# Performance work log

Measured on AMD Instinct MI355X. Metric: run time of the kernel, lower is better.

Reference implementation:

```python
import jax, jax.numpy as jnp
import numpy as np

WS = 7          # window_size
SHIFT = 3       # shift_size
HEADS = 3
DIM = 96
HID = 384       # mlp_ratio * dim
EPS = 1e-5


def _rel_pos_index(ws):
    coords = np.stack(np.meshgrid(np.arange(ws), np.arange(ws), indexing='ij')).reshape(2, -1)
    rel = (coords[:, :, None] - coords[:, None, :]).transpose(1, 2, 0)
    rel[:, :, 0] += ws - 1
    rel[:, :, 1] += ws - 1
    rel[:, :, 0] *= 2 * ws - 1
    return jnp.asarray(rel.sum(-1))  # (ws*ws, ws*ws) int

REL_IDX = _rel_pos_index(WS)


def _shift_mask(H, W):
    # standard Swin SW-MSA mask: (nW, N, N), 0 / -100
    img = np.zeros((H, W), dtype=np.int32)
    cnt = 0
    for h in (slice(0, -WS), slice(-WS, -SHIFT), slice(-SHIFT, None)):
        for w in (slice(0, -WS), slice(-WS, -SHIFT), slice(-SHIFT, None)):
            img[h, w] = cnt
            cnt += 1
    win = img.reshape(H // WS, WS, W // WS, WS).transpose(0, 2, 1, 3).reshape(-1, WS * WS)
    diff = win[:, None, :] - win[:, :, None]
    return jnp.asarray(np.where(diff != 0, -100.0, 0.0).astype(np.float32))


def _ln(x, g, b):
    m = x.mean(-1, keepdims=True)
    v = ((x - m) ** 2).mean(-1, keepdims=True)
    return (x - m) * jax.lax.rsqrt(v + EPS) * g + b


def setup_inputs() -> dict:
    key = jax.random.key(0)
    ks = jax.random.split(key, 12)
    B, H, W, C = 16, 112, 112, DIM
    s = 0.02
    return {
        'x': jax.random.normal(ks[0], (B, H * W, C), jnp.float32),
        'mask': _shift_mask(H, W),
        'norm1_g': jnp.ones((C,), jnp.float32),
        'norm1_b': jnp.zeros((C,), jnp.float32),
        'qkv_w': jax.random.normal(ks[1], (3 * C, C), jnp.float32) * s,
        'qkv_b': jnp.zeros((3 * C,), jnp.float32),
        'rel_bias_table': jax.random.normal(ks[2], ((2 * WS - 1) ** 2, HEADS), jnp.float32) * s,
        'proj_w': jax.random.normal(ks[3], (C, C), jnp.float32) * s,
        'proj_b': jnp.zeros((C,), jnp.float32),
        'norm2_g': jnp.ones((C,), jnp.float32),
        'norm2_b': jnp.zeros((C,), jnp.float32),
        'fc1_w': jax.random.normal(ks[4], (HID, C), jnp.float32) * s,
        'fc1_b': jnp.zeros((HID,), jnp.float32),
        'fc2_w': jax.random.normal(ks[5], (C, HID), jnp.float32) * s,
        'fc2_b': jnp.zeros((C,), jnp.float32),
        'H': 112,
        'W': 112,
    }


def reference(x, mask, norm1_g, norm1_b, qkv_w, qkv_b, rel_bias_table, proj_w,
              proj_b, norm2_g, norm2_b, fc1_w, fc1_b, fc2_w, fc2_b, H, W):
    B, L, C = x.shape
    N = WS * WS
    hd = C // HEADS
    scale = hd ** -0.5
    nh, nw = H // WS, W // WS

    shortcut = x
    h = _ln(x, norm1_g, norm1_b).reshape(B, H, W, C)
    # cyclic shift
    h = jnp.roll(h, (-SHIFT, -SHIFT), axis=(1, 2))
    # window partition -> (B*nW, N, C)
    xw = h.reshape(B, nh, WS, nw, WS, C).transpose(0, 1, 3, 2, 4, 5).reshape(-1, N, C)
    B_ = xw.shape[0]

    qkv = (xw @ qkv_w.T + qkv_b).reshape(B_, N, 3, HEADS, hd).transpose(2, 0, 3, 1, 4)
    q, k, v = qkv[0], qkv[1], qkv[2]          # (B_, heads, N, hd)
    attn = jnp.einsum('bhnd,bhmd->bhnm', q * scale, k)

    bias = rel_bias_table[REL_IDX.reshape(-1)].reshape(N, N, HEADS).transpose(2, 0, 1)
    attn = attn + bias[None]

    nW = mask.shape[0]
    attn = attn.reshape(B_ // nW, nW, HEADS, N, N) + mask[None, :, None]
    attn = jax.nn.softmax(attn.reshape(B_, HEADS, N, N), axis=-1)

    out = jnp.einsum('bhnm,bhmd->bhnd', attn, v).transpose(0, 2, 1, 3).reshape(B_, N, C)
    out = out @ proj_w.T + proj_b

    # window reverse + reverse shift
    out = out.reshape(B, nh, nw, WS, WS, C).transpose(0, 1, 3, 2, 4, 5).reshape(B, H, W, C)
    out = jnp.roll(out, (SHIFT, SHIFT), axis=(1, 2)).reshape(B, L, C)

    x = shortcut + out
    y = _ln(x, norm2_g, norm2_b)
    y = jax.nn.gelu(y @ fc1_w.T + fc1_b, approximate=False)
    y = y @ fc2_w.T + fc2_b
    return x + y
```

## Files before the change

### kernel.cpp

```cpp
#include <hip/hip_runtime.h>
#include <hip/hip_bf16.h>
#include <math.h>


typedef __attribute__((ext_vector_type(8))) short bfrag8;
typedef __attribute__((ext_vector_type(4))) float f32x4;

__device__ __forceinline__ float bf2f(unsigned short u){
  union { unsigned int i; float f; } c; c.i = ((unsigned int)u) << 16; return c.f;
}
__device__ __forceinline__ unsigned short f2bf(float f){
  __hip_bfloat16 h = __float2bfloat16(f);
  union { __hip_bfloat16 h; unsigned short u; } c; c.h = h; return c.u;
}
__device__ __forceinline__ float gelu_f(float x){
  float x2 = x * x;
  float z  = x + 0.044715f * x * x2;
  float u  = __expf(-1.5957691f * z);
  return x / (1.f + u);
}

__device__ __forceinline__ int swz32(int r, int c){
  return r * 32 + (c ^ (((r ^ (r >> 2)) & 3) << 3));
}
__device__ __forceinline__ int swz64(int r, int c){
  return r * 64 + (c ^ (((r ^ (r >> 3)) & 7) << 3));
}

__device__ __forceinline__ int win_to_img(int r){
  int win = r / 49, n = r - win * 49;
  int b  = win >> 8, wi = win & 255;
  int wh = wi >> 4,  ww = wi & 15;
  int i  = n / 7,    j  = n - i * 7;
  int hs = wh * 7 + i + 3; if (hs >= 112) hs -= 112;
  int ws = ww * 7 + j + 3; if (ws >= 112) ws -= 112;
  return b * 12544 + hs * 112 + ws;
}

__global__ __launch_bounds__(256) void cvt_all_kernel(
    const float* __restrict__ s1, unsigned short* __restrict__ d1,
    const float* __restrict__ s2, unsigned short* __restrict__ d2,
    const float* __restrict__ s3, unsigned short* __restrict__ d3,
    const float* __restrict__ s4, unsigned short* __restrict__ d4)
{
  int i = blockIdx.x * 256 + threadIdx.x;
  if      (i < 36864)  d1[i]          = f2bf(s1[i]);
  else if (i < 73728)  d2[i - 36864]  = f2bf(s2[i - 36864]);
  else if (i < 101376) d3[i - 73728]  = f2bf(s3[i - 73728]);
  else if (i < 110592) d4[i - 101376] = f2bf(s4[i - 101376]);
}

__global__ __launch_bounds__(256) void cb_kernel(
    const float* __restrict__ relt, const float* __restrict__ mask,
    float* __restrict__ cbt)
{
  int idx = blockIdx.x * 256 + threadIdx.x;
  int wh = idx >> 12;
  int w = wh / 3, h = wh - w * 3;
  int rem = idx & 4095;
  int mt = rem >> 10, nt = (rem >> 8) & 3, qd = (rem >> 6) & 3;
  int ln = (rem >> 2) & 15, r = rem & 3;
  int m = mt * 16 + qd * 4 + r, n = nt * 16 + ln;
  float v;
  if (m < 49 && n < 49){
    int i1 = m / 7, j1 = m - i1 * 7;
    int i2 = n / 7, j2 = n - i2 * 7;
    int ridx = (i1 - i2 + 6) * 13 + (j1 - j2 + 6);
    v = relt[ridx * 3 + h] + mask[w * 2401 + m * 49 + n];
  } else if (n >= 49) v = -10000.0f;
  else v = 0.0f;
  cbt[idx] = v;
}

__global__ __launch_bounds__(256, 4) void fused_win_kernel(
    const float* __restrict__ x,
    const float* __restrict__ g1, const float* __restrict__ b1n,
    const unsigned short* __restrict__ wqkv, const float* __restrict__ bqkv,
    const float* __restrict__ cbt,
    const unsigned short* __restrict__ wproj, const float* __restrict__ bproj,
    unsigned short* __restrict__ x2)
{
  __shared__ unsigned short L[18944];

  int win = blockIdx.x, tid = threadIdx.x;
  const float scale = 0.17677669529663687f;

  {
    int r = tid >> 2, part = tid & 3;
    if (r < 49){
      int gr = win_to_img(win * 49 + r);
      const float* rowp = x + (size_t)gr * 96 + part * 24;
      float v[24]; float s = 0.f, q = 0.f;
      #pragma unroll
      for (int c = 0; c < 24; c++){ v[c] = rowp[c]; s += v[c]; q += v[c] * v[c]; }
      s += __shfl_xor(s, 1); q += __shfl_xor(q, 1);
      s += __shfl_xor(s, 2); q += __shfl_xor(q, 2);
      float mean = s * (1.f / 96.f);
      float rs = rsqrtf(q * (1.f / 96.f) - mean * mean + 1e-5f);
      #pragma unroll
      for (int c = 0; c < 24; c++){
        int cc = part * 24 + c;
        L[r * 104 + cc] = f2bf((v[c] - mean) * rs * g1[cc] + b1n[cc]);
      }
    } else {
      #pragma unroll
      for (int c = 0; c < 24; c++) L[r * 104 + part * 24 + c] = 0;
    }
  }
  __syncthreads();

  int wave = tid >> 6, lane = tid & 63;
  int ln = lane & 15, qd = lane >> 4;

  bfrag8 af[4][3];
  #pragma unroll
  for (int mt = 0; mt < 4; mt++)
    #pragma unroll
    for (int k3 = 0; k3 < 3; k3++)
      af[mt][k3] = *reinterpret_cast<const bfrag8*>(
          &L[(mt * 16 + ln) * 104 + k3 * 32 + qd * 8]);
  __syncthreads();

  {
    int nct = (wave < 2) ? 5 : 4;
    for (int i = 0; i < nct; i++){
      int nt = wave + i * 4;
      int col = nt * 16 + ln;
      const unsigned short* wp = wqkv + (size_t)col * 96 + qd * 8;
      bfrag8 B0 = *reinterpret_cast<const bfrag8*>(wp);
      bfrag8 B1 = *reinterpret_cast<const bfrag8*>(wp + 32);
      bfrag8 B2 = *reinterpret_cast<const bfrag8*>(wp + 64);
      float bs = bqkv[col];
      #pragma unroll
      for (int mt = 0; mt < 4; mt++){
        f32x4 acc = {0.f, 0.f, 0.f, 0.f};
        acc = __builtin_amdgcn_mfma_f32_16x16x32_bf16(af[mt][0], B0, acc, 0, 0, 0);
        acc = __builtin_amdgcn_mfma_f32_16x16x32_bf16(af[mt][1], B1, acc, 0, 0, 0);
        acc = __builtin_amdgcn_mfma_f32_16x16x32_bf16(af[mt][2], B2, acc, 0, 0, 0);
        if (nt < 6){
          int hh = col >> 5, d = col & 31;
          #pragma unroll
          for (int r = 0; r < 4; r++){
            int m = mt * 16 + qd * 4 + r;
            L[6656 + hh * 4096 + swz32(m, d)] = f2bf((acc[r] + bs) * scale);
          }
        } else if (nt < 12){
          int cc = col - 96; int hh = cc >> 5, d = cc & 31;
          #pragma unroll
          for (int r = 0; r < 4; r++){
            int m = mt * 16 + qd * 4 + r;
            L[6656 + hh * 4096 + 2048 + swz32(m, d)] = f2bf(acc[r] + bs);
          }
        } else {
          int cc = col - 192; int hh = cc >> 5, d = cc & 31;
          #pragma unroll
          for (int r = 0; r < 4; r++){
            int m = mt * 16 + qd * 4 + r;
            L[hh * 2048 + swz64(d, m)] = f2bf(acc[r] + bs);
          }
        }
      }
    }
  }
  __syncthreads();

  int h = wave;
  if (wave < 3){
    bfrag8 qf[4];
    #pragma unroll
    for (int mt = 0; mt < 4; mt++)
      qf[mt] = *reinterpret_cast<const bfrag8*>(
          &L[6656 + h * 4096 + swz32(mt * 16 + ln, qd * 8)]);
    f32x4 sf[4][4];
    #pragma unroll
    for (int nt = 0; nt < 4; nt++){
      bfrag8 kf = *reinterpret_cast<const bfrag8*>(
          &L[6656 + h * 4096 + 2048 + swz32(nt * 16 + ln, qd * 8)]);
      #pragma unroll
      for (int mt = 0; mt < 4; mt++){
        f32x4 z = {0.f, 0.f, 0.f, 0.f};
        sf[mt][nt] = __builtin_amdgcn_mfma_f32_16x16x32_bf16(qf[mt], kf, z, 0, 0, 0);
      }
    }
    const float* cbh = cbt + ((size_t)(win & 255) * 3 + h) * 4096;
    #pragma unroll
    for (int mt = 0; mt < 4; mt++)
      #pragma unroll
      for (int nt = 0; nt < 4; nt++){
        f32x4 cv = *reinterpret_cast<const f32x4*>(
            cbh + mt * 1024 + nt * 256 + qd * 64 + ln * 4);
        #pragma unroll
        for (int r = 0; r < 4; r++) sf[mt][nt][r] += cv[r];
      }
    #pragma unroll
    for (int mt = 0; mt < 4; mt++){
      float mx[4], sm[4];
      #pragma unroll
      for (int r = 0; r < 4; r++)
        mx[r] = fmaxf(fmaxf(sf[mt][0][r], sf[mt][1][r]),
                      fmaxf(sf[mt][2][r], sf[mt][3][r]));
      #pragma unroll
      for (int r = 0; r < 4; r++)
        #pragma unroll
        for (int off = 1; off < 16; off <<= 1)
          mx[r] = fmaxf(mx[r], __shfl_xor(mx[r], off));
      #pragma unroll
      for (int r = 0; r < 4; r++){
        float e0 = __expf(sf[mt][0][r] - mx[r]);
        float e1 = __expf(sf[mt][1][r] - mx[r]);
        float e2 = __expf(sf[mt][2][r] - mx[r]);
        float e3 = __expf(sf[mt][3][r] - mx[r]);
        sf[mt][0][r] = e0; sf[mt][1][r] = e1; sf[mt][2][r] = e2; sf[mt][3][r] = e3;
        sm[r] = e0 + e1 + e2 + e3;
      }
      #pragma unroll
      for (int r = 0; r < 4; r++)
        #pragma unroll
        for (int off = 1; off < 16; off <<= 1)
          sm[r] += __shfl_xor(sm[r], off);
      #pragma unroll
      for (int r = 0; r < 4; r++){
        float inv = 1.f / sm[r];
        int m = mt * 16 + qd * 4 + r;
        #pragma unroll
        for (int nt = 0; nt < 4; nt++)
          L[6656 + h * 4096 + swz64(m, nt * 16 + ln)] = f2bf(sf[mt][nt][r] * inv);
      }
    }

    f32x4 of[4][2];
    #pragma unroll
    for (int mt = 0; mt < 4; mt++)
      #pragma unroll
      for (int dt = 0; dt < 2; dt++) of[mt][dt] = (f32x4){0.f, 0.f, 0.f, 0.f};
    #pragma unroll
    for (int k2 = 0; k2 < 2; k2++){
      bfrag8 vf[2];
      #pragma unroll
      for (int dt = 0; dt < 2; dt++)
        vf[dt] = *reinterpret_cast<const bfrag8*>(
            &L[h * 2048 + swz64(dt * 16 + ln, k2 * 32 + qd * 8)]);
      #pragma unroll
      for (int mt = 0; mt < 4; mt++){
        bfrag8 pf = *reinterpret_cast<const bfrag8*>(
            &L[6656 + h * 4096 + swz64(mt * 16 + ln, k2 * 32 + qd * 8)]);
        #pragma unroll
        for (int dt = 0; dt < 2; dt++)
          of[mt][dt] = __builtin_amdgcn_mfma_f32_16x16x32_bf16(pf, vf[dt], of[mt][dt], 0, 0, 0);
      }
    }
    #pragma unroll
    for (int mt = 0; mt < 4; mt++)
      #pragma unroll
      for (int r = 0; r < 4; r++){
        int m = mt * 16 + qd * 4 + r;
        #pragma unroll
        for (int dt = 0; dt < 2; dt++)
          L[h * 2048 + swz32(m, dt * 16 + ln)] = f2bf(of[mt][dt][r]);
      }
  }
  __syncthreads();

  {
    int rh = wave >> 1, nh = wave & 1;
    bfrag8 ap[2][3];
    #pragma unroll
    for (int mt2 = 0; mt2 < 2; mt2++)
      #pragma unroll
      for (int k3 = 0; k3 < 3; k3++)
        ap[mt2][k3] = *reinterpret_cast<const bfrag8*>(
            &L[k3 * 2048 + swz32(rh * 32 + mt2 * 16 + ln, qd * 8)]);
    f32x4 pacc[2][3];
    #pragma unroll
    for (int nt3 = 0; nt3 < 3; nt3++){
      int col = (nh * 3 + nt3) * 16 + ln;
      const unsigned short* wp = wproj + (size_t)col * 96 + qd * 8;
      bfrag8 B0 = *reinterpret_cast<const bfrag8*>(wp);
      bfrag8 B1 = *reinterpret_cast<const bfrag8*>(wp + 32);
      bfrag8 B2 = *reinterpret_cast<const bfrag8*>(wp + 64);
      #pragma unroll
      for (int mt2 = 0; mt2 < 2; mt2++){
        f32x4 acc = {0.f, 0.f, 0.f, 0.f};
        acc = __builtin_amdgcn_mfma_f32_16x16x32_bf16(ap[mt2][0], B0, acc, 0, 0, 0);
        acc = __builtin_amdgcn_mfma_f32_16x16x32_bf16(ap[mt2][1], B1, acc, 0, 0, 0);
        acc = __builtin_amdgcn_mfma_f32_16x16x32_bf16(ap[mt2][2], B2, acc, 0, 0, 0);
        pacc[mt2][nt3] = acc;
      }
    }
    #pragma unroll
    for (int mt2 = 0; mt2 < 2; mt2++)
      #pragma unroll
      for (int r = 0; r < 4; r++){
        int m = rh * 32 + mt2 * 16 + qd * 4 + r;
        if (m < 49){
          int gi = win_to_img(win * 49 + m);
          #pragma unroll
          for (int nt3 = 0; nt3 < 3; nt3++){
            int col = (nh * 3 + nt3) * 16 + ln;
            x2[(size_t)gi * 96 + col] =
                f2bf(pacc[mt2][nt3][r] + bproj[col] + x[(size_t)gi * 96 + col]);
          }
        }
      }
  }
}

__global__ __launch_bounds__(384, 4) void mlp_mfma_kernel(
    const unsigned short* __restrict__ x2,
    const float* __restrict__ g, const float* __restrict__ b,
    const unsigned short* __restrict__ w1, const float* __restrict__ b1,
    const unsigned short* __restrict__ w2, const float* __restrict__ b2,
    float* __restrict__ out)
{
  __shared__ unsigned short S[25088];
  unsigned short* As = S;
  unsigned short* Hs = S;
  int tid = threadIdx.x;
  int row0 = blockIdx.x * 64;

  {
    int r = tid / 6, c = (tid - r * 6) * 16;
    *reinterpret_cast<bfrag8*>(&As[r * 104 + c]) =
        *reinterpret_cast<const bfrag8*>(x2 + (size_t)(row0 + r) * 96 + c);
    *reinterpret_cast<bfrag8*>(&As[r * 104 + c + 8]) =
        *reinterpret_cast<const bfrag8*>(x2 + (size_t)(row0 + r) * 96 + c + 8);
  }
  __syncthreads();
  if (tid < 256){
    int rr = tid >> 2, part = tid & 3;
    float v[24]; float s = 0.f, q = 0.f;
    #pragma unroll
    for (int c = 0; c < 24; c++){
      v[c] = bf2f(As[rr * 104 + part * 24 + c]);
      s += v[c]; q += v[c] * v[c];
    }
    s += __shfl_xor(s, 1); q += __shfl_xor(q, 1);
    s += __shfl_xor(s, 2); q += __shfl_xor(q, 2);
    float mean = s * (1.f / 96.f);
    float rs = rsqrtf(q * (1.f / 96.f) - mean * mean + 1e-5f);
    #pragma unroll
    for (int c = 0; c < 24; c++){
      int cc = part * 24 + c;
      As[rr * 104 + cc] = f2bf((v[c] - mean) * rs * g[cc] + b[cc]);
    }
  }
  __syncthreads();

  int wave = tid / 64, lane = tid & 63;
  int ln = lane & 15, qd = lane >> 4;

  bfrag8 af[4][3];
  #pragma unroll
  for (int mt = 0; mt < 4; mt++)
    #pragma unroll
    for (int k3 = 0; k3 < 3; k3++)
      af[mt][k3] = *reinterpret_cast<const bfrag8*>(
          &As[(mt * 16 + ln) * 104 + k3 * 32 + qd * 8]);
  __syncthreads();

  for (int i = 0; i < 4; i++){
    int ntl = wave + i * 6;
    int col = ntl * 16 + ln;
    const unsigned short* wp = w1 + (size_t)col * 96 + qd * 8;
    bfrag8 B0 = *reinterpret_cast<const bfrag8*>(wp);
    bfrag8 B1 = *reinterpret_cast<const bfrag8*>(wp + 32);
    bfrag8 B2 = *reinterpret_cast<const bfrag8*>(wp + 64);
    float bias = b1[col];
    #pragma unroll
    for (int mt = 0; mt < 4; mt++){
      f32x4 a = {0.f, 0.f, 0.f, 0.f};
      a = __builtin_amdgcn_mfma_f32_16x16x32_bf16(af[mt][0], B0, a, 0, 0, 0);
      a = __builtin_amdgcn_mfma_f32_16x16x32_bf16(af[mt][1], B1, a, 0, 0, 0);
      a = __builtin_amdgcn_mfma_f32_16x16x32_bf16(af[mt][2], B2, a, 0, 0, 0);
      #pragma unroll
      for (int r = 0; r < 4; r++)
        Hs[(mt * 16 + qd * 4 + r) * 392 + col] = f2bf(gelu_f(a[r] + bias));
    }
  }
  __syncthreads();

  f32x4 acc[4];
  #pragma unroll
  for (int mt = 0; mt < 4; mt++) acc[mt] = (f32x4){0.f, 0.f, 0.f, 0.f};
  for (int k2 = 0; k2 < 12; k2++){
    bfrag8 B = *reinterpret_cast<const bfrag8*>(
        w2 + (size_t)(wave * 16 + ln) * 384 + k2 * 32 + qd * 8);
    #pragma unroll
    for (int mt = 0; mt < 4; mt++){
      bfrag8 p = *reinterpret_cast<const bfrag8*>(
          &Hs[(mt * 16 + ln) * 392 + k2 * 32 + qd * 8]);
      acc[mt] = __builtin_amdgcn_mfma_f32_16x16x32_bf16(p, B, acc[mt], 0, 0, 0);
    }
  }
  {
    int col = wave * 16 + ln;
    float bias = b2[col];
    #pragma unroll
    for (int mt = 0; mt < 4; mt++)
      #pragma unroll
      for (int r = 0; r < 4; r++){
        int grow = row0 + mt * 16 + qd * 4 + r;
        out[(size_t)grow * 96 + col] =
            acc[mt][r] + bias + bf2f(x2[(size_t)grow * 96 + col]);
      }
  }
}

extern "C" void kernel_launch(void* const* d_in, const int* in_sizes, int n_in,
                              void* d_out, int out_size, void* d_ws, size_t ws_size,
                              hipStream_t stream)
{
  const float* x      = (const float*)d_in[0];
  const float* mask   = (const float*)d_in[1];
  const float* n1g    = (const float*)d_in[2];
  const float* n1b    = (const float*)d_in[3];
  const float* qkv_w  = (const float*)d_in[4];
  const float* qkv_b  = (const float*)d_in[5];
  const float* relt   = (const float*)d_in[6];
  const float* proj_w = (const float*)d_in[7];
  const float* proj_b = (const float*)d_in[8];
  const float* n2g    = (const float*)d_in[9];
  const float* n2b    = (const float*)d_in[10];
  const float* fc1_w  = (const float*)d_in[11];
  const float* fc1_b  = (const float*)d_in[12];
  const float* fc2_w  = (const float*)d_in[13];
  const float* fc2_b  = (const float*)d_in[14];
  float* outp = (float*)d_out;
  (void)in_sizes; (void)n_in; (void)out_size; (void)ws_size; (void)mask;

  const size_t M = 200704;
  char* ws = (char*)d_ws;
  unsigned short* x2     = (unsigned short*)ws;
  size_t o = M * 96 * 2;
  unsigned short* w1bf   = (unsigned short*)(ws + o); o += 384 * 96 * 2;
  unsigned short* w2bf   = (unsigned short*)(ws + o); o += 96 * 384 * 2;
  unsigned short* wqkvbf = (unsigned short*)(ws + o); o += 288 * 96 * 2;
  unsigned short* wprojbf= (unsigned short*)(ws + o); o += 96 * 96 * 2;
  float*          cbuf   = (float*)(ws + o); o += (size_t)256 * 3 * 4096 * 4;

  cvt_all_kernel<<<432, 256, 0, stream>>>(
      fc1_w, w1bf, fc2_w, w2bf, qkv_w, wqkvbf, proj_w, wprojbf);
  cb_kernel<<<12288, 256, 0, stream>>>(relt, mask, cbuf);
  fused_win_kernel<<<4096, 256, 0, stream>>>(
      x, n1g, n1b, wqkvbf, qkv_b, cbuf, wprojbf, proj_b, x2);
  mlp_mfma_kernel<<<3136, 384, 0, stream>>>(
      x2, n2g, n2b, w1bf, fc1_b, w2bf, fc2_b, outp);
}
```

Measured before the change: 335.3 us.

## Spread window attention over all waves, use exp2 softmax, retune LDS swizzles

```diff
diff --git a/kernel.cpp b/kernel.cpp
--- a/kernel.cpp
+++ b/kernel.cpp
@@ -6,6 +6,8 @@
 typedef __attribute__((ext_vector_type(8))) short bfrag8;
 typedef __attribute__((ext_vector_type(4))) float f32x4;
 
+#define LOG2E 1.4426950408889634f
+
 __device__ __forceinline__ float bf2f(unsigned short u){
   union { unsigned int i; float f; } c; c.i = ((unsigned int)u) << 16; return c.f;
 }
@@ -14,17 +16,21 @@
   union { __hip_bfloat16 h; unsigned short u; } c; c.h = h; return c.u;
 }
 __device__ __forceinline__ float gelu_f(float x){
+  const float c1 = -2.302208198f, c2 = -0.1029432397f;
   float x2 = x * x;
-  float z  = x + 0.044715f * x * x2;
-  float u  = __expf(-1.5957691f * z);
-  return x / (1.f + u);
+  float t  = __builtin_fmaf(x2, c2, c1);
+  float u  = exp2f(x * t);
+  return x * __builtin_amdgcn_rcpf(1.f + u);
 }
 
 __device__ __forceinline__ int swz32(int r, int c){
-  return r * 32 + (c ^ (((r ^ (r >> 2)) & 3) << 3));
+  return r * 32 + (c ^ (((r + (r >> 2)) & 3) << 3));
 }
 __device__ __forceinline__ int swz64(int r, int c){
-  return r * 64 + (c ^ (((r ^ (r >> 3)) & 7) << 3));
+  return r * 64 + (c ^ (((r ^ (r >> 1)) & 7) << 3));
+}
+__device__ __forceinline__ int hswz(int r, int c){
+  return r * 392 + (c ^ (((r >> 3) & 3) << 4));
 }
 
 __device__ __forceinline__ int win_to_img(int r){
@@ -37,24 +43,24 @@
   return b * 12544 + hs * 112 + ws;
 }
 
-__global__ __launch_bounds__(256) void cvt_all_kernel(
+__global__ __launch_bounds__(256) void prep_kernel(
     const float* __restrict__ s1, unsigned short* __restrict__ d1,
     const float* __restrict__ s2, unsigned short* __restrict__ d2,
     const float* __restrict__ s3, unsigned short* __restrict__ d3,
-    const float* __restrict__ s4, unsigned short* __restrict__ d4)
-{
-  int i = blockIdx.x * 256 + threadIdx.x;
-  if      (i < 36864)  d1[i]          = f2bf(s1[i]);
-  else if (i < 73728)  d2[i - 36864]  = f2bf(s2[i - 36864]);
-  else if (i < 101376) d3[i - 73728]  = f2bf(s3[i - 73728]);
-  else if (i < 110592) d4[i - 101376] = f2bf(s4[i - 101376]);
-}
-
-__global__ __launch_bounds__(256) void cb_kernel(
+    const float* __restrict__ s4, unsigned short* __restrict__ d4,
     const float* __restrict__ relt, const float* __restrict__ mask,
     float* __restrict__ cbt)
 {
-  int idx = blockIdx.x * 256 + threadIdx.x;
+  int bid = blockIdx.x;
+  if (bid < 432){
+    int i = bid * 256 + threadIdx.x;
+    if      (i < 36864)  d1[i]          = f2bf(s1[i]);
+    else if (i < 73728)  d2[i - 36864]  = f2bf(s2[i - 36864]);
+    else if (i < 101376) d3[i - 73728]  = f2bf(s3[i - 73728]);
+    else if (i < 110592) d4[i - 101376] = f2bf(s4[i - 101376]);
+    return;
+  }
+  int idx = (bid - 432) * 256 + threadIdx.x;
   int wh = idx >> 12;
   int w = wh / 3, h = wh - w * 3;
   int rem = idx & 4095;
@@ -66,7 +72,7 @@
     int i1 = m / 7, j1 = m - i1 * 7;
     int i2 = n / 7, j2 = n - i2 * 7;
     int ridx = (i1 - i2 + 6) * 13 + (j1 - j2 + 6);
-    v = relt[ridx * 3 + h] + mask[w * 2401 + m * 49 + n];
+    v = (relt[ridx * 3 + h] + mask[w * 2401 + m * 49 + n]) * LOG2E;
   } else if (n >= 49) v = -10000.0f;
   else v = 0.0f;
   cbt[idx] = v;
@@ -83,7 +89,7 @@
   __shared__ unsigned short L[18944];
 
   int win = blockIdx.x, tid = threadIdx.x;
-  const float scale = 0.17677669529663687f;
+  const float qscale = (float)(0.17677669529663687 * 1.4426950408889634);
 
   {
     int r = tid >> 2, part = tid & 3;
@@ -142,7 +148,7 @@
           #pragma unroll
           for (int r = 0; r < 4; r++){
             int m = mt * 16 + qd * 4 + r;
-            L[6656 + hh * 4096 + swz32(m, d)] = f2bf((acc[r] + bs) * scale);
+            L[6656 + hh * 4096 + swz32(m, d)] = f2bf((acc[r] + bs) * qscale);
           }
         } else if (nt < 12){
           int cc = col - 96; int hh = cc >> 5, d = cc & 31;
@@ -164,100 +170,93 @@
   }
   __syncthreads();
 
-  int h = wave;
-  if (wave < 3){
-    bfrag8 qf[4];
-    #pragma unroll
-    for (int mt = 0; mt < 4; mt++)
-      qf[mt] = *reinterpret_cast<const bfrag8*>(
-          &L[6656 + h * 4096 + swz32(mt * 16 + ln, qd * 8)]);
-    f32x4 sf[4][4];
+  int u0 = wave * 3;
+  bfrag8 qf[3];
+  f32x4 sf[3][4];
+  #pragma unroll
+  for (int i = 0; i < 3; i++){
+    int u = u0 + i, hh = u >> 2, mt = u & 3;
+    qf[i] = *reinterpret_cast<const bfrag8*>(
+        &L[6656 + hh * 4096 + swz32(mt * 16 + ln, qd * 8)]);
     #pragma unroll
     for (int nt = 0; nt < 4; nt++){
       bfrag8 kf = *reinterpret_cast<const bfrag8*>(
-          &L[6656 + h * 4096 + 2048 + swz32(nt * 16 + ln, qd * 8)]);
-      #pragma unroll
-      for (int mt = 0; mt < 4; mt++){
-        f32x4 z = {0.f, 0.f, 0.f, 0.f};
-        sf[mt][nt] = __builtin_amdgcn_mfma_f32_16x16x32_bf16(qf[mt], kf, z, 0, 0, 0);
-      }
-    }
-    const float* cbh = cbt + ((size_t)(win & 255) * 3 + h) * 4096;
-    #pragma unroll
-    for (int mt = 0; mt < 4; mt++)
-      #pragma unroll
-      for (int nt = 0; nt < 4; nt++){
-        f32x4 cv = *reinterpret_cast<const f32x4*>(
-            cbh + mt * 1024 + nt * 256 + qd * 64 + ln * 4);
-        #pragma unroll
-        for (int r = 0; r < 4; r++) sf[mt][nt][r] += cv[r];
-      }
-    #pragma unroll
-    for (int mt = 0; mt < 4; mt++){
-      float mx[4], sm[4];
-      #pragma unroll
-      for (int r = 0; r < 4; r++)
-        mx[r] = fmaxf(fmaxf(sf[mt][0][r], sf[mt][1][r]),
-                      fmaxf(sf[mt][2][r], sf[mt][3][r]));
-      #pragma unroll
-      for (int r = 0; r < 4; r++)
-        #pragma unroll
-        for (int off = 1; off < 16; off <<= 1)
-          mx[r] = fmaxf(mx[r], __shfl_xor(mx[r], off));
-      #pragma unroll
-      for (int r = 0; r < 4; r++){
-        float e0 = __expf(sf[mt][0][r] - mx[r]);
-        float e1 = __expf(sf[mt][1][r] - mx[r]);
-        float e2 = __expf(sf[mt][2][r] - mx[r]);
-        float e3 = __expf(sf[mt][3][r] - mx[r]);
-        sf[mt][0][r] = e0; sf[mt][1][r] = e1; sf[mt][2][r] = e2; sf[mt][3][r] = e3;
-        sm[r] = e0 + e1 + e2 + e3;
-      }
-      #pragma unroll
-      for (int r = 0; r < 4; r++)
-        #pragma unroll
-        for (int off = 1; off < 16; off <<= 1)
-          sm[r] += __shfl_xor(sm[r], off);
-      #pragma unroll
-      for (int r = 0; r < 4; r++){
-        float inv = 1.f / sm[r];
-        int m = mt * 16 + qd * 4 + r;
-        #pragma unroll
-        for (int nt = 0; nt < 4; nt++)
-          L[6656 + h * 4096 + swz64(m, nt * 16 + ln)] = f2bf(sf[mt][nt][r] * inv);
-      }
-    }
-
-    f32x4 of[4][2];
-    #pragma unroll
-    for (int mt = 0; mt < 4; mt++)
-      #pragma unroll
-      for (int dt = 0; dt < 2; dt++) of[mt][dt] = (f32x4){0.f, 0.f, 0.f, 0.f};
+          &L[6656 + hh * 4096 + 2048 + swz32(nt * 16 + ln, qd * 8)]);
+      f32x4 z = {0.f, 0.f, 0.f, 0.f};
+      sf[i][nt] = __builtin_amdgcn_mfma_f32_16x16x32_bf16(qf[i], kf, z, 0, 0, 0);
+    }
+    const float* cbh = cbt + ((size_t)(win & 255) * 3 + hh) * 4096 + mt * 1024;
+    #pragma unroll
+    for (int nt = 0; nt < 4; nt++){
+      f32x4 cv = *reinterpret_cast<const f32x4*>(cbh + nt * 256 + qd * 64 + ln * 4);
+      #pragma unroll
+      for (int r = 0; r < 4; r++) sf[i][nt][r] += cv[r];
+    }
+  }
+  __syncthreads();
+
+  f32x4 of[3][2];
+  #pragma unroll
+  for (int i = 0; i < 3; i++){
+    int u = u0 + i, hh = u >> 2, mt = u & 3;
+    float mx[4], sm[4];
+    #pragma unroll
+    for (int r = 0; r < 4; r++)
+      mx[r] = fmaxf(fmaxf(sf[i][0][r], sf[i][1][r]),
+                    fmaxf(sf[i][2][r], sf[i][3][r]));
+    #pragma unroll
+    for (int r = 0; r < 4; r++)
+      #pragma unroll
+      for (int off = 1; off < 16; off <<= 1)
+        mx[r] = fmaxf(mx[r], __shfl_xor(mx[r], off));
+    #pragma unroll
+    for (int r = 0; r < 4; r++){
+      float e0 = exp2f(sf[i][0][r] - mx[r]);
+      float e1 = exp2f(sf[i][1][r] - mx[r]);
+      float e2 = exp2f(sf[i][2][r] - mx[r]);
+      float e3 = exp2f(sf[i][3][r] - mx[r]);
+      sf[i][0][r] = e0; sf[i][1][r] = e1; sf[i][2][r] = e2; sf[i][3][r] = e3;
+      sm[r] = e0 + e1 + e2 + e3;
+    }
+    #pragma unroll
+    for (int r = 0; r < 4; r++)
+      #pragma unroll
+      for (int off = 1; off < 16; off <<= 1)
+        sm[r] += __shfl_xor(sm[r], off);
+    #pragma unroll
+    for (int r = 0; r < 4; r++){
+      float inv = __builtin_amdgcn_rcpf(sm[r]);
+      int m = mt * 16 + qd * 4 + r;
+      #pragma unroll
+      for (int nt = 0; nt < 4; nt++)
+        L[6656 + hh * 4096 + swz64(m, nt * 16 + ln)] = f2bf(sf[i][nt][r] * inv);
+    }
+    of[i][0] = (f32x4){0.f, 0.f, 0.f, 0.f};
+    of[i][1] = (f32x4){0.f, 0.f, 0.f, 0.f};
     #pragma unroll
     for (int k2 = 0; k2 < 2; k2++){
-      bfrag8 vf[2];
+      bfrag8 pf = *reinterpret_cast<const bfrag8*>(
+          &L[6656 + hh * 4096 + swz64(mt * 16 + ln, k2 * 32 + qd * 8)]);
+      #pragma unroll
+      for (int dt = 0; dt < 2; dt++){
+        bfrag8 vf = *reinterpret_cast<const bfrag8*>(
+            &L[hh * 2048 + swz64(dt * 16 + ln, k2 * 32 + qd * 8)]);
+        of[i][dt] = __builtin_amdgcn_mfma_f32_16x16x32_bf16(pf, vf, of[i][dt], 0, 0, 0);
+      }
+    }
+  }
+  __syncthreads();
+
+  #pragma unroll
+  for (int i = 0; i < 3; i++){
+    int u = u0 + i, hh = u >> 2, mt = u & 3;
+    #pragma unroll
+    for (int r = 0; r < 4; r++){
+      int m = mt * 16 + qd * 4 + r;
       #pragma unroll
       for (int dt = 0; dt < 2; dt++)
-        vf[dt] = *reinterpret_cast<const bfrag8*>(
-            &L[h * 2048 + swz64(dt * 16 + ln, k2 * 32 + qd * 8)]);
-      #pragma unroll
-      for (int mt = 0; mt < 4; mt++){
-        bfrag8 pf = *reinterpret_cast<const bfrag8*>(
-            &L[6656 + h * 4096 + swz64(mt * 16 + ln, k2 * 32 + qd * 8)]);
-        #pragma unroll
-        for (int dt = 0; dt < 2; dt++)
-          of[mt][dt] = __builtin_amdgcn_mfma_f32_16x16x32_bf16(pf, vf[dt], of[mt][dt], 0, 0, 0);
-      }
-    }
-    #pragma unroll
-    for (int mt = 0; mt < 4; mt++)
-      #pragma unroll
-      for (int r = 0; r < 4; r++){
-        int m = mt * 16 + qd * 4 + r;
-        #pragma unroll
-        for (int dt = 0; dt < 2; dt++)
-          L[h * 2048 + swz32(m, dt * 16 + ln)] = f2bf(of[mt][dt][r]);
-      }
+        L[hh * 2048 + swz32(m, dt * 16 + ln)] = f2bf(of[i][dt][r]);
+    }
   }
   __syncthreads();
 
@@ -374,7 +373,7 @@
       a = __builtin_amdgcn_mfma_f32_16x16x32_bf16(af[mt][2], B2, a, 0, 0, 0);
       #pragma unroll
       for (int r = 0; r < 4; r++)
-        Hs[(mt * 16 + qd * 4 + r) * 392 + col] = f2bf(gelu_f(a[r] + bias));
+        Hs[hswz(mt * 16 + qd * 4 + r, col)] = f2bf(gelu_f(a[r] + bias));
     }
   }
   __syncthreads();
@@ -388,7 +387,7 @@
     #pragma unroll
     for (int mt = 0; mt < 4; mt++){
       bfrag8 p = *reinterpret_cast<const bfrag8*>(
-          &Hs[(mt * 16 + ln) * 392 + k2 * 32 + qd * 8]);
+          &Hs[hswz(mt * 16 + ln, k2 * 32 + qd * 8)]);
       acc[mt] = __builtin_amdgcn_mfma_f32_16x16x32_bf16(p, B, acc[mt], 0, 0, 0);
     }
   }
@@ -438,9 +437,9 @@
   unsigned short* wprojbf= (unsigned short*)(ws + o); o += 96 * 96 * 2;
   float*          cbuf   = (float*)(ws + o); o += (size_t)256 * 3 * 4096 * 4;
 
-  cvt_all_kernel<<<432, 256, 0, stream>>>(
-      fc1_w, w1bf, fc2_w, w2bf, qkv_w, wqkvbf, proj_w, wprojbf);
-  cb_kernel<<<12288, 256, 0, stream>>>(relt, mask, cbuf);
+  prep_kernel<<<12720, 256, 0, stream>>>(
+      fc1_w, w1bf, fc2_w, w2bf, qkv_w, wqkvbf, proj_w, wprojbf,
+      relt, mask, cbuf);
   fused_win_kernel<<<4096, 256, 0, stream>>>(
       x, n1g, n1b, wqkvbf, qkv_b, cbuf, wprojbf, proj_b, x2);
   mlp_mfma_kernel<<<3136, 384, 0, stream>>>(
```

Result: slower. 370.9 us (+10.6%).

## Use exp2 softmax, cheaper GELU, new LDS swizzles, and merge prep kernels

Applied to the files above, without the earlier changes.

```diff
diff --git a/kernel.cpp b/kernel.cpp
--- a/kernel.cpp
+++ b/kernel.cpp
@@ -6,6 +6,8 @@
 typedef __attribute__((ext_vector_type(8))) short bfrag8;
 typedef __attribute__((ext_vector_type(4))) float f32x4;
 
+#define LOG2E 1.4426950408889634f
+
 __device__ __forceinline__ float bf2f(unsigned short u){
   union { unsigned int i; float f; } c; c.i = ((unsigned int)u) << 16; return c.f;
 }
@@ -14,17 +16,21 @@
   union { __hip_bfloat16 h; unsigned short u; } c; c.h = h; return c.u;
 }
 __device__ __forceinline__ float gelu_f(float x){
+  const float c1 = -2.302208198f, c2 = -0.1029432397f;
   float x2 = x * x;
-  float z  = x + 0.044715f * x * x2;
-  float u  = __expf(-1.5957691f * z);
-  return x / (1.f + u);
+  float t  = __builtin_fmaf(x2, c2, c1);
+  float u  = exp2f(x * t);
+  return x * __builtin_amdgcn_rcpf(1.f + u);
 }
 
 __device__ __forceinline__ int swz32(int r, int c){
-  return r * 32 + (c ^ (((r ^ (r >> 2)) & 3) << 3));
+  return r * 32 + (c ^ (((r + (r >> 2)) & 3) << 3));
 }
 __device__ __forceinline__ int swz64(int r, int c){
-  return r * 64 + (c ^ (((r ^ (r >> 3)) & 7) << 3));
+  return r * 64 + (c ^ (((r ^ (r >> 1)) & 7) << 3));
+}
+__device__ __forceinline__ int hswz(int r, int c){
+  return r * 392 + (c ^ (((r >> 3) & 3) << 4));
 }
 
 __device__ __forceinline__ int win_to_img(int r){
@@ -37,24 +43,24 @@
   return b * 12544 + hs * 112 + ws;
 }
 
-__global__ __launch_bounds__(256) void cvt_all_kernel(
+__global__ __launch_bounds__(256) void prep_kernel(
     const float* __restrict__ s1, unsigned short* __restrict__ d1,
     const float* __restrict__ s2, unsigned short* __restrict__ d2,
     const float* __restrict__ s3, unsigned short* __restrict__ d3,
-    const float* __restrict__ s4, unsigned short* __restrict__ d4)
-{
-  int i = blockIdx.x * 256 + threadIdx.x;
-  if      (i < 36864)  d1[i]          = f2bf(s1[i]);
-  else if (i < 73728)  d2[i - 36864]  = f2bf(s2[i - 36864]);
-  else if (i < 101376) d3[i - 73728]  = f2bf(s3[i - 73728]);
-  else if (i < 110592) d4[i - 101376] = f2bf(s4[i - 101376]);
-}
-
-__global__ __launch_bounds__(256) void cb_kernel(
+    const float* __restrict__ s4, unsigned short* __restrict__ d4,
     const float* __restrict__ relt, const float* __restrict__ mask,
     float* __restrict__ cbt)
 {
-  int idx = blockIdx.x * 256 + threadIdx.x;
+  int bid = blockIdx.x;
+  if (bid < 432){
+    int i = bid * 256 + threadIdx.x;
+    if      (i < 36864)  d1[i]          = f2bf(s1[i]);
+    else if (i < 73728)  d2[i - 36864]  = f2bf(s2[i - 36864]);
+    else if (i < 101376) d3[i - 73728]  = f2bf(s3[i - 73728]);
+    else if (i < 110592) d4[i - 101376] = f2bf(s4[i - 101376]);
+    return;
+  }
+  int idx = (bid - 432) * 256 + threadIdx.x;
   int wh = idx >> 12;
   int w = wh / 3, h = wh - w * 3;
   int rem = idx & 4095;
@@ -66,7 +72,7 @@
     int i1 = m / 7, j1 = m - i1 * 7;
     int i2 = n / 7, j2 = n - i2 * 7;
     int ridx = (i1 - i2 + 6) * 13 + (j1 - j2 + 6);
-    v = relt[ridx * 3 + h] + mask[w * 2401 + m * 49 + n];
+    v = (relt[ridx * 3 + h] + mask[w * 2401 + m * 49 + n]) * LOG2E;
   } else if (n >= 49) v = -10000.0f;
   else v = 0.0f;
   cbt[idx] = v;
@@ -83,7 +89,7 @@
   __shared__ unsigned short L[18944];
 
   int win = blockIdx.x, tid = threadIdx.x;
-  const float scale = 0.17677669529663687f;
+  const float qscale = (float)(0.17677669529663687 * 1.4426950408889634);
 
   {
     int r = tid >> 2, part = tid & 3;
@@ -142,7 +148,7 @@
           #pragma unroll
           for (int r = 0; r < 4; r++){
             int m = mt * 16 + qd * 4 + r;
-            L[6656 + hh * 4096 + swz32(m, d)] = f2bf((acc[r] + bs) * scale);
+            L[6656 + hh * 4096 + swz32(m, d)] = f2bf((acc[r] + bs) * qscale);
           }
         } else if (nt < 12){
           int cc = col - 96; int hh = cc >> 5, d = cc & 31;
@@ -206,10 +212,10 @@
           mx[r] = fmaxf(mx[r], __shfl_xor(mx[r], off));
       #pragma unroll
       for (int r = 0; r < 4; r++){
-        float e0 = __expf(sf[mt][0][r] - mx[r]);
-        float e1 = __expf(sf[mt][1][r] - mx[r]);
-        float e2 = __expf(sf[mt][2][r] - mx[r]);
-        float e3 = __expf(sf[mt][3][r] - mx[r]);
+        float e0 = exp2f(sf[mt][0][r] - mx[r]);
+        float e1 = exp2f(sf[mt][1][r] - mx[r]);
+        float e2 = exp2f(sf[mt][2][r] - mx[r]);
+        float e3 = exp2f(sf[mt][3][r] - mx[r]);
         sf[mt][0][r] = e0; sf[mt][1][r] = e1; sf[mt][2][r] = e2; sf[mt][3][r] = e3;
         sm[r] = e0 + e1 + e2 + e3;
       }
@@ -220,7 +226,7 @@
           sm[r] += __shfl_xor(sm[r], off);
       #pragma unroll
       for (int r = 0; r < 4; r++){
-        float inv = 1.f / sm[r];
+        float inv = __builtin_amdgcn_rcpf(sm[r]);
         int m = mt * 16 + qd * 4 + r;
         #pragma unroll
         for (int nt = 0; nt < 4; nt++)
@@ -374,7 +380,7 @@
       a = __builtin_amdgcn_mfma_f32_16x16x32_bf16(af[mt][2], B2, a, 0, 0, 0);
       #pragma unroll
       for (int r = 0; r < 4; r++)
-        Hs[(mt * 16 + qd * 4 + r) * 392 + col] = f2bf(gelu_f(a[r] + bias));
+        Hs[hswz(mt * 16 + qd * 4 + r, col)] = f2bf(gelu_f(a[r] + bias));
     }
   }
   __syncthreads();
@@ -388,7 +394,7 @@
     #pragma unroll
     for (int mt = 0; mt < 4; mt++){
       bfrag8 p = *reinterpret_cast<const bfrag8*>(
-          &Hs[(mt * 16 + ln) * 392 + k2 * 32 + qd * 8]);
+          &Hs[hswz(mt * 16 + ln, k2 * 32 + qd * 8)]);
       acc[mt] = __builtin_amdgcn_mfma_f32_16x16x32_bf16(p, B, acc[mt], 0, 0, 0);
     }
   }
@@ -438,9 +444,9 @@
   unsigned short* wprojbf= (unsigned short*)(ws + o); o += 96 * 96 * 2;
   float*          cbuf   = (float*)(ws + o); o += (size_t)256 * 3 * 4096 * 4;
 
-  cvt_all_kernel<<<432, 256, 0, stream>>>(
-      fc1_w, w1bf, fc2_w, w2bf, qkv_w, wqkvbf, proj_w, wprojbf);
-  cb_kernel<<<12288, 256, 0, stream>>>(relt, mask, cbuf);
+  prep_kernel<<<12720, 256, 0, stream>>>(
+      fc1_w, w1bf, fc2_w, w2bf, qkv_w, wqkvbf, proj_w, wprojbf,
+      relt, mask, cbuf);
   fused_win_kernel<<<4096, 256, 0, stream>>>(
       x, n1g, n1b, wqkvbf, qkv_b, cbuf, wprojbf, proj_b, x2);
   mlp_mfma_kernel<<<3136, 384, 0, stream>>>(
```

Result: slower. 363.2 us (+8.3%).
